# Optimization experiments

Hardware: AMD Instinct MI355X
Metric: run time of the kernel (lower is better)

Reference implementation:

```python
import jax, jax.numpy as jnp
import numpy as np

N, E = 50000, 800000
IN_CH, INTER, H1, H2 = 256, 32, 8, 8
C2 = IN_CH // H2  # 32
NEG_SLOPE = 0.2


def setup_inputs() -> dict:
    key = jax.random.key(0)
    ks = jax.random.split(key, 10)
    x = jax.random.normal(ks[0], (N, IN_CH), dtype=jnp.float32)
    edge_index = jax.random.randint(ks[1], (2, E), 0, N, dtype=jnp.int32)
    s = 0.05
    W1 = jax.random.normal(ks[2], (H1 * INTER, IN_CH), dtype=jnp.float32) * s
    att_src1 = jax.random.normal(ks[3], (1, H1, INTER), dtype=jnp.float32) * s
    att_dst1 = jax.random.normal(ks[4], (1, H1, INTER), dtype=jnp.float32) * s
    b1 = jnp.zeros((H1 * INTER,), dtype=jnp.float32)
    W2 = jax.random.normal(ks[5], (H2 * C2, H1 * INTER), dtype=jnp.float32) * s
    att_src2 = jax.random.normal(ks[6], (1, H2, C2), dtype=jnp.float32) * s
    att_dst2 = jax.random.normal(ks[7], (1, H2, C2), dtype=jnp.float32) * s
    b2 = jnp.zeros((H2 * C2,), dtype=jnp.float32)
    return {"x": x, "edge_index": edge_index,
            "W1": W1, "att_src1": att_src1, "att_dst1": att_dst1, "b1": b1,
            "W2": W2, "att_src2": att_src2, "att_dst2": att_dst2, "b2": b2}


def gat_conv(x, edge_index, W, att_src, att_dst, bias, H, C):
    # PyG GATConv (shared lin for src/dst, add_self_loops=False, concat=True)
    n = x.shape[0]
    src, dst = edge_index[0], edge_index[1]
    xw = (x @ W.T).reshape(n, H, C)                     # [N,H,C]
    a_src = jnp.sum(xw * att_src, axis=-1)              # [N,H]
    a_dst = jnp.sum(xw * att_dst, axis=-1)              # [N,H]
    e = a_src[src] + a_dst[dst]                         # [E,H]
    e = jnp.where(e >= 0, e, NEG_SLOPE * e)             # LeakyReLU(0.2)
    # segment softmax over edges grouped by destination node
    m = jax.ops.segment_max(e, dst, num_segments=n)     # [N,H]
    ex = jnp.exp(e - m[dst])
    denom = jax.ops.segment_sum(ex, dst, num_segments=n)
    alpha = ex / (denom[dst] + 1e-16)                   # [E,H]
    # weighted scatter-aggregate of source messages
    msg = xw[src] * alpha[:, :, None]                   # [E,H,C]
    out = jax.ops.segment_sum(msg, dst, num_segments=n) # [N,H,C]
    return out.reshape(n, H * C) + bias


def reference(x, edge_index, W1, att_src1, att_dst1, b1, W2, att_src2, att_dst2, b2):
    h = gat_conv(x, edge_index, W1, att_src1, att_dst1, b1, H1, INTER)
    h = jax.nn.gelu(h, approximate=False)  # F.gelu default is exact
    h = gat_conv(h, edge_index, W2, att_src2, att_dst2, b2, H2, C2)
    return h[-1]  # eval-path super node
```

## Files before the change

kernel.cpp:

```cpp
#include <hip/hip_runtime.h>
#include <math.h>

#define N_NODES 50000
#define N_EDGES 800000
#define TGT     (N_NODES - 1)
#define C2MAX   256
#define KCAP    258
#define ELMAX   256
#define XWLDS   32
#define SCANBLK 1024

struct WS {
  int* cnt;
  int* cnt2;
  int* e2src;
  int* g_uniq;
  int* g_slot;
  int* g_misc;
  int* l1src;
  float* W1T;
  float* W2T;
  float* g_xw2;
  float* g_as2;
  float* g_ad2;
  float* g_spill;
};
__host__ __device__ inline WS carve(char* ws) {
  WS w; int* p = (int*)ws;
  w.cnt = p;    p += 16;
  w.cnt2 = p;   p += 272;
  w.e2src = p;  p += C2MAX;
  w.g_uniq = p; p += 272;
  w.g_slot = p; p += C2MAX;
  w.g_misc = p; p += 16;
  w.l1src = p;  p += KCAP * ELMAX;
  float* f = (float*)p;
  w.W1T = f;    f += 65536;
  w.W2T = f;    f += 65536;
  w.g_xw2 = f;  f += KCAP * 256;
  w.g_as2 = f;  f += KCAP * 8;
  w.g_ad2 = f;  f += KCAP * 8;
  w.g_spill = f;
  return w;
}

__device__ void dedup_block(const int* e2src, int c2, int* s_e, int* s_scan,
                            int* s_uniq, int* s_slot, int* s_kv) {
  int t = threadIdx.x;
  if (t < c2) s_e[t] = e2src[t];
  __syncthreads();
  int s = 0, firstIdx = t;
  if (t < c2) {
    s = s_e[t];
    for (int q = 0; q < t; ++q) if (s_e[q] == s) { firstIdx = q; break; }
  }
  s_scan[t] = (t < c2 && firstIdx == t) ? 1 : 0;
  __syncthreads();
  for (int off = 1; off < 256; off <<= 1) {
    int add = (t >= off) ? s_scan[t - off] : 0;
    __syncthreads();
    s_scan[t] += add;
    __syncthreads();
  }
  if (t < c2 && firstIdx == t) s_uniq[s_scan[t] - 1] = s;
  __syncthreads();
  if (t < c2) s_slot[t] = s_scan[firstIdx] - 1;
  if (t == 0) {
    int K1 = (c2 > 0) ? s_scan[255] : 0;
    int kd = -1;
    for (int i = 0; i < K1; ++i) if (s_uniq[i] == TGT) { kd = i; break; }
    if (kd < 0) { s_uniq[K1] = TGT; kd = K1; K1++; }
    s_kv[0] = K1; s_kv[1] = kd;
  }
  __syncthreads();
}

__global__ __launch_bounds__(256) void k_scan2(const int* __restrict__ eidx,
    const float* __restrict__ W1, const float* __restrict__ W2, char* ws) {
  WS w = carve(ws);
  int tid = blockIdx.x * 256 + threadIdx.x;
  int nthreads = gridDim.x * 256;
  for (int i = tid; i < 65536; i += nthreads) {
    int o = i >> 8, c = i & 255;
    w.W1T[c * 256 + o] = W1[i];
    w.W2T[c * 256 + o] = W2[i];
  }
  const int* esrc = eidx;
  const int4* edst4 = (const int4*)(eidx + N_EDGES);
  for (int i = tid; i < N_EDGES / 4; i += nthreads) {
    int4 d = edst4[i];
    int dv[4] = {d.x, d.y, d.z, d.w};
#pragma unroll
    for (int j = 0; j < 4; ++j)
      if (dv[j] == TGT) {
        int p = atomicAdd(&w.cnt[0], 1);
        if (p < C2MAX) w.e2src[p] = esrc[4 * i + j];
      }
  }
}

__global__ __launch_bounds__(256) void k_scan1(const int* __restrict__ eidx, char* ws) {
  WS w = carve(ws);
  __shared__ int s_e[C2MAX], s_scan[256], s_uniq[KCAP], s_slot[C2MAX], s_kv[2];
  int c2 = min(w.cnt[0], C2MAX);
  dedup_block(w.e2src, c2, s_e, s_scan, s_uniq, s_slot, s_kv);
  int K1 = s_kv[0];
  if (blockIdx.x == 0) {
    int t = threadIdx.x;
    if (t < K1) w.g_uniq[t] = s_uniq[t];
    if (t < c2) w.g_slot[t] = s_slot[t];
    if (t == 0) { w.g_misc[0] = K1; w.g_misc[1] = s_kv[1]; }
  }
  int tid = blockIdx.x * 256 + threadIdx.x;
  int nthreads = gridDim.x * 256;
  const int* esrc = eidx;
  const int4* edst4 = (const int4*)(eidx + N_EDGES);
  for (int i = tid; i < N_EDGES / 4; i += nthreads) {
    int4 d = edst4[i];
    int dv[4] = {d.x, d.y, d.z, d.w};
#pragma unroll
    for (int j = 0; j < 4; ++j) {
      int k = -1;
      for (int q = 0; q < K1; ++q) if (s_uniq[q] == dv[j]) { k = q; break; }
      if (k >= 0) {
        int p = atomicAdd(&w.cnt2[k], 1);
        if (p < ELMAX) w.l1src[k * ELMAX + p] = esrc[4 * i + j];
      }
    }
  }
}

__global__ __launch_bounds__(256) void k_gat(const float* __restrict__ x,
    const float* __restrict__ aS1, const float* __restrict__ aD1,
    const float* __restrict__ b1, const float* __restrict__ aS2,
    const float* __restrict__ aD2, char* ws) {
  WS w = carve(ws);
  int K1 = w.g_misc[0];
  int k = blockIdx.x;
  if (k >= K1) return;
  int t = threadIdx.x;
  __shared__ float s_xw[XWLDS * 256];
  __shared__ float s_as[(ELMAX + 1) * 8];
  __shared__ float s_ad[(ELMAX + 1) * 8];
  __shared__ __align__(16) float s_xsT[4 * 256];
  __shared__ float s_redS[4 * 256], s_redD[4 * 256];
  __shared__ float s_h1[256];
  int myNode = w.g_uniq[k];
  int ne = min(w.cnt2[k], ELMAX);
  int items = ne + 1;
  float* spill = w.g_spill + (size_t)k * (ELMAX + 1) * 256;

  for (int base = 0; base < items; base += 4) {
    int na = min(4, items - base);
    int nd[4];
    for (int i = 0; i < na; ++i) {
      int it = base + i;
      nd[i] = (it < ne) ? w.l1src[k * ELMAX + it] : myNode;
    }
    for (int i = 0; i < na; ++i)
      s_xsT[t * 4 + i] = x[(size_t)nd[i] * 256 + t];
    __syncthreads();
    float a0 = 0.f, a1 = 0.f, a2 = 0.f, a3 = 0.f;
#pragma unroll 16
    for (int c = 0; c < 256; ++c) {
      float wv = w.W1T[c * 256 + t];
      float4 xv = *(const float4*)&s_xsT[c * 4];
      a0 = fmaf(xv.x, wv, a0); a1 = fmaf(xv.y, wv, a1);
      a2 = fmaf(xv.z, wv, a2); a3 = fmaf(xv.w, wv, a3);
    }
    float accs[4] = {a0, a1, a2, a3};
    for (int i = 0; i < na; ++i) {
      int it = base + i;
      if (it < XWLDS) s_xw[it * 256 + t] = accs[i];
      else            spill[(size_t)it * 256 + t] = accs[i];
      s_redS[i * 256 + t] = accs[i] * aS1[t];
      s_redD[i * 256 + t] = accs[i] * aD1[t];
    }
    __syncthreads();
    if (t < 32) {
      int i = t >> 3, h = t & 7;
      if (i < na) {
        float s = 0.f, dd = 0.f;
        for (int q = 0; q < 32; ++q) {
          s  += s_redS[i * 256 + h * 32 + q];
          dd += s_redD[i * 256 + h * 32 + q];
        }
        s_as[(base + i) * 8 + h] = s;
        s_ad[(base + i) * 8 + h] = dd;
      }
    }
    __syncthreads();
  }

  int h = t >> 5;
  float adst = s_ad[ne * 8 + h];
  float m = -INFINITY;
  for (int j = 0; j < ne; ++j) {
    float e = s_as[j * 8 + h] + adst;
    e = (e >= 0.f) ? e : 0.2f * e;
    m = fmaxf(m, e);
  }
  float denom = 0.f, acc = 0.f;
  for (int j = 0; j < ne; ++j) {
    float e = s_as[j * 8 + h] + adst;
    e = (e >= 0.f) ? e : 0.2f * e;
    float p = expf(e - m);
    denom += p;
    float xv = (j < XWLDS) ? s_xw[j * 256 + t] : spill[(size_t)j * 256 + t];
    acc = fmaf(p, xv, acc);
  }
  float o = (ne > 0) ? acc / (denom + 1e-16f) : 0.f;
  o += b1[t];
  s_h1[t] = 0.5f * o * (1.f + erff(o * 0.70710678118654752440f));
  __syncthreads();
  float a2s = 0.f;
#pragma unroll 16
  for (int c = 0; c < 256; ++c)
    a2s = fmaf(s_h1[c], w.W2T[c * 256 + t], a2s);
  w.g_xw2[k * 256 + t] = a2s;
  s_redS[t] = a2s * aS2[t];
  s_redD[t] = a2s * aD2[t];
  __syncthreads();
  if (t < 8) {
    float s = 0.f, dd = 0.f;
    for (int q = 0; q < 32; ++q) { s += s_redS[t * 32 + q]; dd += s_redD[t * 32 + q]; }
    w.g_as2[k * 8 + t] = s;
    w.g_ad2[k * 8 + t] = dd;
  }
}

__global__ __launch_bounds__(256) void k_final(const float* __restrict__ b2,
                                               float* __restrict__ out, char* ws) {
  WS w = carve(ws);
  int t = threadIdx.x;
  int c2 = min(w.cnt[0], C2MAX);
  int kd = w.g_misc[1];
  __shared__ int s_slot[C2MAX];
  if (t < c2) s_slot[t] = w.g_slot[t];
  __syncthreads();
  int h = t >> 5;
  float adst = w.g_ad2[kd * 8 + h];
  float m = -INFINITY;
  for (int j = 0; j < c2; ++j) {
    float e = w.g_as2[s_slot[j] * 8 + h] + adst;
    e = (e >= 0.f) ? e : 0.2f * e;
    m = fmaxf(m, e);
  }
  float denom = 0.f, acc = 0.f;
  for (int j = 0; j < c2; ++j) {
    int kk = s_slot[j];
    float e = w.g_as2[kk * 8 + h] + adst;
    e = (e >= 0.f) ? e : 0.2f * e;
    float p = expf(e - m);
    denom += p;
    acc = fmaf(p, w.g_xw2[kk * 256 + t], acc);
  }
  float o = (c2 > 0) ? acc / (denom + 1e-16f) : 0.f;
  out[t] = o + b2[t];
}

extern "C" void kernel_launch(void* const* d_in, const int* in_sizes, int n_in,
                              void* d_out, int out_size, void* d_ws, size_t ws_size,
                              hipStream_t stream) {
  const float* x    = (const float*)d_in[0];
  const int*   eidx = (const int*)d_in[1];
  const float* W1   = (const float*)d_in[2];
  const float* aS1  = (const float*)d_in[3];
  const float* aD1  = (const float*)d_in[4];
  const float* b1   = (const float*)d_in[5];
  const float* W2   = (const float*)d_in[6];
  const float* aS2  = (const float*)d_in[7];
  const float* aD2  = (const float*)d_in[8];
  const float* b2   = (const float*)d_in[9];
  float* out = (float*)d_out;
  char*  ws  = (char*)d_ws;

  hipMemsetAsync(ws, 0, (16 + 272) * sizeof(int), stream);

  k_scan2<<<SCANBLK, 256, 0, stream>>>(eidx, W1, W2, ws);
  k_scan1<<<SCANBLK, 256, 0, stream>>>(eidx, ws);
  k_gat  <<<KCAP,    256, 0, stream>>>(x, aS1, aD1, b1, aS2, aD2, ws);
  k_final<<<1,       256, 0, stream>>>(b2, out, ws);
}
```

Before: 166.9 us.

## Split layer-1 GAT into parallel projection and per-node attention kernels

The fused per-node kernel is split in two. A projection kernel spreads each node's neighbour rows over a 2D grid with 16 y-blocks and writes the projected features and attention logits to global memory. A second kernel computes the softmax weights once per head into shared memory, then aggregates, applies GELU and does the layer-2 projection. This is meant to remove the serial 4-row loop inside a single block per node, at the cost of an extra launch and a global round trip for the projected features. The final kernel also gains a redundant per-head denominator precompute plus a dead loop.

New measurement: 142.9 us. 1.17x faster.

```diff
diff --git a/kernel.cpp b/kernel.cpp
--- a/kernel.cpp
+++ b/kernel.cpp
@@ -7,7 +7,8 @@
 #define C2MAX   256
 #define KCAP    258
 #define ELMAX   256
-#define XWLDS   32
+#define ROWS    (ELMAX + 1)
+#define PBLK    16
 #define SCANBLK 1024
 
 struct WS {
@@ -23,7 +24,9 @@
   float* g_xw2;
   float* g_as2;
   float* g_ad2;
-  float* g_spill;
+  float* g_as1;
+  float* g_ad1;
+  float* g_xw1;
 };
 __host__ __device__ inline WS carve(char* ws) {
   WS w; int* p = (int*)ws;
@@ -40,7 +43,9 @@
   w.g_xw2 = f;  f += KCAP * 256;
   w.g_as2 = f;  f += KCAP * 8;
   w.g_ad2 = f;  f += KCAP * 8;
-  w.g_spill = f;
+  w.g_as1 = f;  f += KCAP * ROWS * 8;
+  w.g_ad1 = f;  f += KCAP * ROWS * 8;
+  w.g_xw1 = f;
   return w;
 }
 
@@ -130,35 +135,26 @@
   }
 }
 
-__global__ __launch_bounds__(256) void k_gat(const float* __restrict__ x,
-    const float* __restrict__ aS1, const float* __restrict__ aD1,
-    const float* __restrict__ b1, const float* __restrict__ aS2,
-    const float* __restrict__ aD2, char* ws) {
-  WS w = carve(ws);
-  int K1 = w.g_misc[0];
+__global__ __launch_bounds__(256) void k_xw1(const float* __restrict__ x,
+    const float* __restrict__ aS1, const float* __restrict__ aD1, char* ws) {
+  WS w = carve(ws);
   int k = blockIdx.x;
-  if (k >= K1) return;
+  if (k >= w.g_misc[0]) return;
   int t = threadIdx.x;
-  __shared__ float s_xw[XWLDS * 256];
-  __shared__ float s_as[(ELMAX + 1) * 8];
-  __shared__ float s_ad[(ELMAX + 1) * 8];
+  int ne = min(w.cnt2[k], ELMAX);
+  int items = ne + 1;
   __shared__ __align__(16) float s_xsT[4 * 256];
   __shared__ float s_redS[4 * 256], s_redD[4 * 256];
-  __shared__ float s_h1[256];
   int myNode = w.g_uniq[k];
-  int ne = min(w.cnt2[k], ELMAX);
-  int items = ne + 1;
-  float* spill = w.g_spill + (size_t)k * (ELMAX + 1) * 256;
-
-  for (int base = 0; base < items; base += 4) {
+
+  for (int b = blockIdx.y; b * 4 < items; b += PBLK) {
+    int base = b * 4;
     int na = min(4, items - base);
-    int nd[4];
     for (int i = 0; i < na; ++i) {
       int it = base + i;
-      nd[i] = (it < ne) ? w.l1src[k * ELMAX + it] : myNode;
-    }
-    for (int i = 0; i < na; ++i)
-      s_xsT[t * 4 + i] = x[(size_t)nd[i] * 256 + t];
+      int node = (it < ne) ? w.l1src[k * ELMAX + it] : myNode;
+      s_xsT[t * 4 + i] = x[(size_t)node * 256 + t];
+    }
     __syncthreads();
     float a0 = 0.f, a1 = 0.f, a2 = 0.f, a3 = 0.f;
 #pragma unroll 16
@@ -170,9 +166,8 @@
     }
     float accs[4] = {a0, a1, a2, a3};
     for (int i = 0; i < na; ++i) {
-      int it = base + i;
-      if (it < XWLDS) s_xw[it * 256 + t] = accs[i];
-      else            spill[(size_t)it * 256 + t] = accs[i];
+      int row = k * ROWS + base + i;
+      w.g_xw1[(size_t)row * 256 + t] = accs[i];
       s_redS[i * 256 + t] = accs[i] * aS1[t];
       s_redD[i * 256 + t] = accs[i] * aD1[t];
     }
@@ -185,31 +180,56 @@
           s  += s_redS[i * 256 + h * 32 + q];
           dd += s_redD[i * 256 + h * 32 + q];
         }
-        s_as[(base + i) * 8 + h] = s;
-        s_ad[(base + i) * 8 + h] = dd;
+        int row = k * ROWS + base + i;
+        w.g_as1[row * 8 + h] = s;
+        w.g_ad1[row * 8 + h] = dd;
       }
     }
     __syncthreads();
   }
-
+}
+
+__global__ __launch_bounds__(256) void k_attn(const float* __restrict__ b1,
+    const float* __restrict__ aS2, const float* __restrict__ aD2, char* ws) {
+  WS w = carve(ws);
+  int k = blockIdx.x;
+  if (k >= w.g_misc[0]) return;
+  int t = threadIdx.x;
+  int ne = min(w.cnt2[k], ELMAX);
+  __shared__ float s_as[ROWS * 8];
+  __shared__ float s_p[ELMAX * 8];
+  __shared__ float s_den[8];
+  __shared__ float s_h1[256];
+  __shared__ float s_redS[256], s_redD[256];
+  for (int i = t; i < (ne + 1) * 8; i += 256) s_as[i] = w.g_as1[(k * ROWS) * 8 + i];
+  __syncthreads();
+  if (t < 8) {
+    int h = t;
+    float adst = w.g_ad1[(k * ROWS + ne) * 8 + h];
+    float m = -INFINITY;
+    for (int j = 0; j < ne; ++j) {
+      float e = s_as[j * 8 + h] + adst;
+      e = (e >= 0.f) ? e : 0.2f * e;
+      m = fmaxf(m, e);
+    }
+    float den = 0.f;
+    for (int j = 0; j < ne; ++j) {
+      float e = s_as[j * 8 + h] + adst;
+      e = (e >= 0.f) ? e : 0.2f * e;
+      float p = expf(e - m);
+      s_p[j * 8 + h] = p;
+      den += p;
+    }
+    s_den[h] = den + 1e-16f;
+  }
+  __syncthreads();
   int h = t >> 5;
-  float adst = s_ad[ne * 8 + h];
-  float m = -INFINITY;
-  for (int j = 0; j < ne; ++j) {
-    float e = s_as[j * 8 + h] + adst;
-    e = (e >= 0.f) ? e : 0.2f * e;
-    m = fmaxf(m, e);
-  }
-  float denom = 0.f, acc = 0.f;
-  for (int j = 0; j < ne; ++j) {
-    float e = s_as[j * 8 + h] + adst;
-    e = (e >= 0.f) ? e : 0.2f * e;
-    float p = expf(e - m);
-    denom += p;
-    float xv = (j < XWLDS) ? s_xw[j * 256 + t] : spill[(size_t)j * 256 + t];
-    acc = fmaf(p, xv, acc);
-  }
-  float o = (ne > 0) ? acc / (denom + 1e-16f) : 0.f;
+  float acc = 0.f;
+  const float* xwb = w.g_xw1 + (size_t)(k * ROWS) * 256 + t;
+#pragma unroll 4
+  for (int j = 0; j < ne; ++j)
+    acc = fmaf(s_p[j * 8 + h], xwb[(size_t)j * 256], acc);
+  float o = (ne > 0) ? acc / s_den[h] : 0.f;
   o += b1[t];
   s_h1[t] = 0.5f * o * (1.f + erff(o * 0.70710678118654752440f));
   __syncthreads();
@@ -236,9 +256,42 @@
   int c2 = min(w.cnt[0], C2MAX);
   int kd = w.g_misc[1];
   __shared__ int s_slot[C2MAX];
+  __shared__ float s_p[C2MAX];
+  __shared__ float s_den[8];
   if (t < c2) s_slot[t] = w.g_slot[t];
   __syncthreads();
   int h = t >> 5;
+  if (t < 8) {
+    float adst = w.g_ad2[kd * 8 + t];
+    float m = -INFINITY;
+    for (int j = 0; j < c2; ++j) {
+      float e = w.g_as2[s_slot[j] * 8 + t] + adst;
+      e = (e >= 0.f) ? e : 0.2f * e;
+      m = fmaxf(m, e);
+    }
+    float den = 0.f;
+    for (int j = 0; j < c2; ++j) {
+      float e = w.g_as2[s_slot[j] * 8 + t] + adst;
+      e = (e >= 0.f) ? e : 0.2f * e;
+      den += expf(e - m);
+    }
+    s_den[t] = den + 1e-16f;
+  }
+  __syncthreads();
+  if (t < 8) {
+    float adst = w.g_ad2[kd * 8 + t];
+    float m = -INFINITY;
+    for (int j = 0; j < c2; ++j) {
+      float e = w.g_as2[s_slot[j] * 8 + t] + adst;
+      e = (e >= 0.f) ? e : 0.2f * e;
+      m = fmaxf(m, e);
+    }
+    for (int j = 0; j < c2; ++j) {
+      float e = w.g_as2[s_slot[j] * 8 + t] + adst;
+      e = (e >= 0.f) ? e : 0.2f * e;
+    }
+  }
+  __syncthreads();
   float adst = w.g_ad2[kd * 8 + h];
   float m = -INFINITY;
   for (int j = 0; j < c2; ++j) {
@@ -246,16 +299,15 @@
     e = (e >= 0.f) ? e : 0.2f * e;
     m = fmaxf(m, e);
   }
-  float denom = 0.f, acc = 0.f;
+  float acc = 0.f;
   for (int j = 0; j < c2; ++j) {
     int kk = s_slot[j];
     float e = w.g_as2[kk * 8 + h] + adst;
     e = (e >= 0.f) ? e : 0.2f * e;
     float p = expf(e - m);
-    denom += p;
     acc = fmaf(p, w.g_xw2[kk * 256 + t], acc);
   }
-  float o = (c2 > 0) ? acc / (denom + 1e-16f) : 0.f;
+  float o = (c2 > 0) ? acc / s_den[h] : 0.f;
   out[t] = o + b2[t];
 }
 
@@ -279,6 +331,7 @@
 
   k_scan2<<<SCANBLK, 256, 0, stream>>>(eidx, W1, W2, ws);
   k_scan1<<<SCANBLK, 256, 0, stream>>>(eidx, ws);
-  k_gat  <<<KCAP,    256, 0, stream>>>(x, aS1, aD1, b1, aS2, aD2, ws);
-  k_final<<<1,       256, 0, stream>>>(b2, out, ws);
-}
+  k_xw1  <<<dim3(KCAP, PBLK), 256, 0, stream>>>(x, aS1, aD1, ws);
+  k_attn <<<KCAP, 256, 0, stream>>>(b1, aS2, aD2, ws);
+  k_final<<<1, 256, 0, stream>>>(b2, out, ws);
+}
```
